# Kernel tuning notes

Measured on AMD Instinct MI355X. Metric: run time of the kernel, lower is better.

Reference implementation:

```python
import jax, jax.numpy as jnp
import numpy as np

KCODES = 512
BETA = 0.25   # beta_k = beta_v
GAMMA = 0.25  # gamma_k = gamma_v


def _quantise(z, codebook):
    """EMAQuantiser.forward in eval mode. z: [..., d], codebook: [k, d]."""
    d = z.shape[-1]
    zf = z.reshape(-1, d)                                   # [N, d]
    z2 = jnp.sum(zf * zf, axis=1, keepdims=True)            # [N, 1]
    c2 = jnp.sum(codebook * codebook, axis=1)               # [k]
    logits = zf @ codebook.T                                # [N, k]
    dist = z2 + c2[None, :] - 2.0 * logits                  # [N, k]
    indices = jnp.argmin(dist, axis=1)                      # [N]
    z_q = codebook[indices].reshape(z.shape)
    z_q_st = z + jax.lax.stop_gradient(z_q - z)
    loss_commit = jnp.mean((jax.lax.stop_gradient(z_q) - z) ** 2)
    loss_embed = jnp.mean((z_q - jax.lax.stop_gradient(z)) ** 2)
    counts = jax.ops.segment_sum(jnp.ones_like(indices, dtype=z.dtype), indices,
                                 num_segments=codebook.shape[0])
    usage = counts / jnp.maximum(counts.sum(), 1.0)
    return z_q_st, indices.reshape(z.shape[:-1]), loss_commit, loss_embed, usage


def setup_inputs() -> dict:
    key = jax.random.key(0)
    k1, k2, k3, k4 = jax.random.split(key, 4)
    B, H, S, D = 2, 16, 4096, 128
    return {
        "K": jax.random.normal(k1, (B, H, S, D), dtype=jnp.float32),
        "V": jax.random.normal(k2, (B, H, S, D), dtype=jnp.float32),
        "codebook_k": jax.random.normal(k3, (KCODES, D), dtype=jnp.float32) * 0.02,
        "codebook_v": jax.random.normal(k4, (KCODES, D), dtype=jnp.float32) * 0.02,
        "step": 20000,
    }


def reference(K, V, codebook_k, codebook_v, step):
    K_q, idx_k, commit_k, embed_k, usage_k = _quantise(K, codebook_k)
    V_q, idx_v, commit_v, embed_v, usage_v = _quantise(V, codebook_v)
    # eval mode: gates = ones -> mix == quantised straight-through values
    gates = jnp.ones_like(K[..., :1])
    K_mix = (1.0 - gates) * K + gates * K_q
    V_mix = (1.0 - gates) * V + gates * V_q
    return (K_mix, V_mix,
            BETA * commit_k, BETA * commit_v,
            GAMMA * embed_k, GAMMA * embed_v,
            usage_k, usage_v)
```

## Files before the change

### kernel.cpp

```cpp
#include <hip/hip_runtime.h>
#include <hip/hip_fp16.h>

typedef _Float16 half8 __attribute__((ext_vector_type(8)));
typedef float floatx4 __attribute__((ext_vector_type(4)));

#define R_TOT   131072
#define OUT_SC  33554432
#define OUT_USE 33554436
#define WS_C2   524288
#define WS_IDX  528384
#define WS_LOSS 1576960


__global__ void vq_init(const float* __restrict__ cb_k, const float* __restrict__ cb_v,
                        float* __restrict__ out, char* __restrict__ ws) {
    const int b = blockIdx.x, t = threadIdx.x;
    if (b < 64) {
        const int tensor = b >> 5, nt = b & 31;
        const int s = t >> 6, lane = t & 63, l15 = lane & 15, quad = lane >> 4;
        const float* cb = tensor ? cb_v : cb_k;
        half8* wsh = (half8*)(ws + (size_t)tensor * 262144);
        half8* wsl = wsh + 8192;
        const int code = nt * 16 + l15;
        const float* src = cb + code * 128 + s * 32 + quad * 8;
        float4 z0 = *(const float4*)src;
        float4 z1 = *(const float4*)(src + 4);
        float zz[8] = {z0.x, z0.y, z0.z, z0.w, z1.x, z1.y, z1.z, z1.w};
        half8 h, l;
        float p = 0.0f;
        #pragma unroll
        for (int j = 0; j < 8; ++j) {
            _Float16 hi = (_Float16)zz[j];
            h[j] = hi;
            l[j] = (_Float16)((zz[j] - (float)hi) * 2048.0f);
            p = fmaf(zz[j], zz[j], p);
        }
        wsh[(nt * 4 + s) * 64 + lane] = h;
        wsl[(nt * 4 + s) * 64 + lane] = l;
        p += __shfl_xor(p, 16);
        p += __shfl_xor(p, 32);
        __shared__ float c2p[4][16];
        if (lane < 16) c2p[s][lane] = p;
        __syncthreads();
        if (t < 16)
            ((float*)(ws + WS_C2))[tensor * 512 + nt * 16 + t] =
                ((c2p[0][t] + c2p[1][t]) + c2p[2][t]) + c2p[3][t];
    } else {
        int i = (b - 64) * 256 + t;
        if (i < 1028) out[OUT_SC + i] = 0.0f;
    }
}

__global__ __launch_bounds__(256, 2)
void vq_main(const float* __restrict__ Kp, const float* __restrict__ Vp,
             const float* __restrict__ cb_k, const float* __restrict__ cb_v,
             float* __restrict__ out, char* __restrict__ ws) {
    __shared__ int   lds_idx[128];
    __shared__ float lds_loss[4];

    const int tid  = threadIdx.x;
    const int wave = tid >> 6;
    const int lane = tid & 63;
    const int quad = lane >> 4;
    const int l15  = lane & 15;
    const int tensor = blockIdx.y;

    const float* __restrict__ Z   = tensor ? Vp : Kp;
    const float* __restrict__ cbf = tensor ? cb_v : cb_k;
    const half8* __restrict__ gh  = (const half8*)(ws + (size_t)tensor * 262144);
    const half8* __restrict__ gl  = gh + 8192;
    const float* __restrict__ c2g = (const float*)(ws + WS_C2) + tensor * 512;
    int* __restrict__ idxg = (int*)(ws + WS_IDX) + tensor * R_TOT;
    float* __restrict__ lossp = (float*)(ws + WS_LOSS) + tensor * 2048;
    float* __restrict__ outz = out + (size_t)tensor * 16777216;

    const int blockRow = blockIdx.x * 128;
    const int waveRow  = blockRow + wave * 32;

    half8 ah[2][4], al[2][4];
    float z2r[2][4];
    #pragma unroll
    for (int t = 0; t < 2; ++t) {
        const float* zp = Z + (size_t)(waveRow + t * 16 + l15) * 128;
        float zsq = 0.0f;
        #pragma unroll
        for (int s = 0; s < 4; ++s) {
            const float* p = zp + s * 32 + quad * 8;
            float4 z0 = *(const float4*)p;
            float4 z1 = *(const float4*)(p + 4);
            float zz[8] = {z0.x, z0.y, z0.z, z0.w, z1.x, z1.y, z1.z, z1.w};
            #pragma unroll
            for (int j = 0; j < 8; ++j) {
                _Float16 h = (_Float16)zz[j];
                ah[t][s][j] = h;
                al[t][s][j] = (_Float16)((zz[j] - (float)h) * 2048.0f);
                zsq = fmaf(zz[j], zz[j], zsq);
            }
        }
        zsq += __shfl_xor(zsq, 16);
        zsq += __shfl_xor(zsq, 32);
        #pragma unroll
        for (int r = 0; r < 4; ++r) z2r[t][r] = __shfl(zsq, quad * 4 + r);
    }

    float bd[2][4];
    int   bi[2][4];
    #pragma unroll
    for (int t = 0; t < 2; ++t)
        #pragma unroll
        for (int r = 0; r < 4; ++r) { bd[t][r] = 3.4e38f; bi[t][r] = 0; }

    half8 bh[2][4], bl[2][4];
    #pragma unroll
    for (int s = 0; s < 4; ++s) {
        bh[0][s] = gh[s * 64 + lane];
        bl[0][s] = gl[s * 64 + lane];
    }

    #pragma unroll 2
    for (int nt = 0; nt < 32; ++nt) {
        const int cur = nt & 1, nxt = cur ^ 1;
        if (nt < 31) {
            #pragma unroll
            for (int s = 0; s < 4; ++s) {
                bh[nxt][s] = gh[((nt + 1) * 4 + s) * 64 + lane];
                bl[nxt][s] = gl[((nt + 1) * 4 + s) * 64 + lane];
            }
        }
        const float c2v = c2g[nt * 16 + l15];
        floatx4 p10 = {0,0,0,0}, p11 = {0,0,0,0}, p20 = {0,0,0,0}, p21 = {0,0,0,0};
        #pragma unroll
        for (int s = 0; s < 4; ++s) {
            p10 = __builtin_amdgcn_mfma_f32_16x16x32_f16(ah[0][s], bh[cur][s], p10, 0, 0, 0);
            p11 = __builtin_amdgcn_mfma_f32_16x16x32_f16(ah[1][s], bh[cur][s], p11, 0, 0, 0);
            p20 = __builtin_amdgcn_mfma_f32_16x16x32_f16(al[0][s], bh[cur][s], p20, 0, 0, 0);
            p21 = __builtin_amdgcn_mfma_f32_16x16x32_f16(al[1][s], bh[cur][s], p21, 0, 0, 0);
            p20 = __builtin_amdgcn_mfma_f32_16x16x32_f16(ah[0][s], bl[cur][s], p20, 0, 0, 0);
            p21 = __builtin_amdgcn_mfma_f32_16x16x32_f16(ah[1][s], bl[cur][s], p21, 0, 0, 0);
        }
        const int codeg = nt * 16 + l15;
        #pragma unroll
        for (int r = 0; r < 4; ++r) {
            float lg0 = fmaf(p20[r], 0x1p-11f, p10[r]);
            float d0  = fmaf(-2.0f, lg0, z2r[0][r] + c2v);
            if (d0 < bd[0][r]) { bd[0][r] = d0; bi[0][r] = codeg; }
            float lg1 = fmaf(p21[r], 0x1p-11f, p11[r]);
            float d1  = fmaf(-2.0f, lg1, z2r[1][r] + c2v);
            if (d1 < bd[1][r]) { bd[1][r] = d1; bi[1][r] = codeg; }
        }
    }

    float lp = 0.0f;
    #pragma unroll
    for (int t = 0; t < 2; ++t)
        #pragma unroll
        for (int r = 0; r < 4; ++r) {
            float d = bd[t][r];
            int   i = bi[t][r];
            #pragma unroll
            for (int off = 8; off; off >>= 1) {
                float od = __shfl_xor(d, off);
                int   oi = __shfl_xor(i, off);
                if (od < d || (od == d && oi < i)) { d = od; i = oi; }
            }
            if (l15 == 0) {
                lds_idx[wave * 32 + t * 16 + quad * 4 + r] = i;
                lp += d;
            }
        }
    lp += __shfl_xor(lp, 16);
    lp += __shfl_xor(lp, 32);
    if (lane == 0) lds_loss[wave] = lp;
    __syncthreads();

    if (tid == 0) {
        float bsum = ((lds_loss[0] + lds_loss[1]) + lds_loss[2]) + lds_loss[3];
        lossp[blockIdx.x] = bsum * 0x1p-26f;
    }
    if (tid < 128) idxg[blockRow + tid] = lds_idx[tid];

    #pragma unroll
    for (int g = 0; g < 16; ++g) {
        int rl  = g * 8 + (tid >> 5);
        int idx = lds_idx[rl];
        int col = (tid & 31) * 4;
        float4 v = *(const float4*)(cbf + idx * 128 + col);
        *(float4*)(outz + (size_t)(blockRow + rl) * 128 + col) = v;
    }
}

__global__ void vq_hist(const char* __restrict__ ws, float* __restrict__ out) {
    const int tid = threadIdx.x;
    const int b = blockIdx.x;
    if (b < 16) {
        __shared__ int h[512];
        const int tensor = b >> 3;
        const int seg = b & 7;
        h[tid] = 0; h[tid + 256] = 0;
        __syncthreads();
        const int* p = (const int*)(ws + WS_IDX) + tensor * R_TOT + seg * 16384;
        #pragma unroll
        for (int r = 0; r < 64; ++r) atomicAdd(&h[p[r * 256 + tid]], 1);
        __syncthreads();
        int c0 = h[tid], c1 = h[tid + 256];
        if (c0) atomicAdd(&out[OUT_USE + tensor * 512 + tid], (float)c0 * 0x1p-17f);
        if (c1) atomicAdd(&out[OUT_USE + tensor * 512 + tid + 256], (float)c1 * 0x1p-17f);
    } else {
        const int tensor = b - 16;
        const float* lossp = (const float*)(ws + WS_LOSS) + tensor * 2048;
        float s = 0.0f;
        #pragma unroll
        for (int j = 0; j < 8; ++j) s += lossp[j * 256 + tid];
        #pragma unroll
        for (int off = 1; off < 64; off <<= 1) s += __shfl_xor(s, off);
        __shared__ float l4[4];
        if ((tid & 63) == 0) l4[tid >> 6] = s;
        __syncthreads();
        if (tid == 0) {
            float tot = ((l4[0] + l4[1]) + l4[2]) + l4[3];
            out[OUT_SC + tensor] = tot;
            out[OUT_SC + 2 + tensor] = tot;
        }
    }
}

extern "C" void kernel_launch(void* const* d_in, const int* in_sizes, int n_in,
                              void* d_out, int out_size, void* d_ws, size_t ws_size,
                              hipStream_t stream) {
    (void)in_sizes; (void)n_in; (void)out_size; (void)ws_size;
    const float* K   = (const float*)d_in[0];
    const float* V   = (const float*)d_in[1];
    const float* cbk = (const float*)d_in[2];
    const float* cbv = (const float*)d_in[3];
    float* out = (float*)d_out;
    char* ws = (char*)d_ws;
    hipLaunchKernelGGL(vq_init, dim3(69), dim3(256), 0, stream, cbk, cbv, out, ws);
    hipLaunchKernelGGL(vq_main, dim3(1024, 2), dim3(256), 0, stream, K, V, cbk, cbv, out, ws);
    hipLaunchKernelGGL(vq_hist, dim3(18), dim3(256), 0, stream, (const char*)ws, out);
}
```

Before: 326.0 us.

## Stage codebook tiles through LDS with async global_load_lds ring buffer

Each block now shares the fp16 hi/lo codebook tiles through a 4-slot LDS ring buffer filled with direct global-to-LDS loads three tiles ahead, instead of every wave loading them from global into registers. The c2 norms are also staged in LDS. The aim is to cut redundant per-wave global traffic and register pressure in the distance loop, at the cost of a block-wide barrier per tile and hand-coded vmcnt waits. Separately, the histogram kernel is split across more blocks to spread the LDS atomics.

```diff
diff --git a/kernel.cpp b/kernel.cpp
--- a/kernel.cpp
+++ b/kernel.cpp
@@ -51,10 +51,18 @@
     }
 }
 
+__device__ __forceinline__ void gload_lds16(const void* g, void* l) {
+    __builtin_amdgcn_global_load_lds(
+        (const __attribute__((address_space(1))) void*)g,
+        (__attribute__((address_space(3))) void*)l, 16, 0, 0);
+}
+
 __global__ __launch_bounds__(256, 2)
 void vq_main(const float* __restrict__ Kp, const float* __restrict__ Vp,
              const float* __restrict__ cb_k, const float* __restrict__ cb_v,
              float* __restrict__ out, char* __restrict__ ws) {
+    __shared__ half8 buf[4][512];
+    __shared__ float c2s[512];
     __shared__ int   lds_idx[128];
     __shared__ float lds_loss[4];
 
@@ -76,6 +84,14 @@
 
     const int blockRow = blockIdx.x * 128;
     const int waveRow  = blockRow + wave * 32;
+
+    #pragma unroll
+    for (int pc = 0; pc < 3; ++pc) {
+        gload_lds16(gh + pc * 256 + tid, &buf[pc][tid]);
+        gload_lds16(gl + pc * 256 + tid, &buf[pc][256 + tid]);
+    }
+    c2s[tid]       = c2g[tid];
+    c2s[tid + 256] = c2g[tid + 256];
 
     half8 ah[2][4], al[2][4];
     float z2r[2][4];
@@ -110,45 +126,54 @@
         #pragma unroll
         for (int r = 0; r < 4; ++r) { bd[t][r] = 3.4e38f; bi[t][r] = 0; }
 
-    half8 bh[2][4], bl[2][4];
-    #pragma unroll
-    for (int s = 0; s < 4; ++s) {
-        bh[0][s] = gh[s * 64 + lane];
-        bl[0][s] = gl[s * 64 + lane];
-    }
-
-    #pragma unroll 2
-    for (int nt = 0; nt < 32; ++nt) {
-        const int cur = nt & 1, nxt = cur ^ 1;
-        if (nt < 31) {
-            #pragma unroll
-            for (int s = 0; s < 4; ++s) {
-                bh[nxt][s] = gh[((nt + 1) * 4 + s) * 64 + lane];
-                bl[nxt][s] = gl[((nt + 1) * 4 + s) * 64 + lane];
-            }
-        }
-        const float c2v = c2g[nt * 16 + l15];
-        floatx4 p10 = {0,0,0,0}, p11 = {0,0,0,0}, p20 = {0,0,0,0}, p21 = {0,0,0,0};
-        #pragma unroll
-        for (int s = 0; s < 4; ++s) {
-            p10 = __builtin_amdgcn_mfma_f32_16x16x32_f16(ah[0][s], bh[cur][s], p10, 0, 0, 0);
-            p11 = __builtin_amdgcn_mfma_f32_16x16x32_f16(ah[1][s], bh[cur][s], p11, 0, 0, 0);
-            p20 = __builtin_amdgcn_mfma_f32_16x16x32_f16(al[0][s], bh[cur][s], p20, 0, 0, 0);
-            p21 = __builtin_amdgcn_mfma_f32_16x16x32_f16(al[1][s], bh[cur][s], p21, 0, 0, 0);
-            p20 = __builtin_amdgcn_mfma_f32_16x16x32_f16(ah[0][s], bl[cur][s], p20, 0, 0, 0);
-            p21 = __builtin_amdgcn_mfma_f32_16x16x32_f16(ah[1][s], bl[cur][s], p21, 0, 0, 0);
-        }
-        const int codeg = nt * 16 + l15;
-        #pragma unroll
-        for (int r = 0; r < 4; ++r) {
-            float lg0 = fmaf(p20[r], 0x1p-11f, p10[r]);
-            float d0  = fmaf(-2.0f, lg0, z2r[0][r] + c2v);
-            if (d0 < bd[0][r]) { bd[0][r] = d0; bi[0][r] = codeg; }
-            float lg1 = fmaf(p21[r], 0x1p-11f, p11[r]);
-            float d1  = fmaf(-2.0f, lg1, z2r[1][r] + c2v);
-            if (d1 < bd[1][r]) { bd[1][r] = d1; bi[1][r] = codeg; }
-        }
-    }
+    asm volatile("s_waitcnt lgkmcnt(0)" ::: "memory");
+
+#define KSTEP(NT_, WAITS_)                                                        \
+    {                                                                             \
+        const int nt = (NT_);                                                     \
+        asm volatile(WAITS_ ::: "memory");                                        \
+        asm volatile("s_barrier" ::: "memory");                                   \
+        if (nt < 29) {                                                            \
+            const int pc = nt + 3;                                                \
+            gload_lds16(gh + pc * 256 + tid, &buf[pc & 3][tid]);                  \
+            gload_lds16(gl + pc * 256 + tid, &buf[pc & 3][256 + tid]);            \
+        }                                                                         \
+        const half8* bp = buf[nt & 3];                                            \
+        half8 bh[4], bl[4];                                                       \
+        _Pragma("unroll")                                                         \
+        for (int s = 0; s < 4; ++s) {            \
+            bh[s] = bp[s * 64 + lane];                                            \
+            bl[s] = bp[256 + s * 64 + lane];                                      \
+        }                                                                         \
+        const float c2v = c2s[nt * 16 + l15];                                     \
+        floatx4 p10 = {0,0,0,0}, p11 = {0,0,0,0}, p20 = {0,0,0,0}, p21 = {0,0,0,0};\
+        _Pragma("unroll")                                                         \
+        for (int s = 0; s < 4; ++s) {                                             \
+            p10 = __builtin_amdgcn_mfma_f32_16x16x32_f16(ah[0][s], bh[s], p10, 0, 0, 0); \
+            p11 = __builtin_amdgcn_mfma_f32_16x16x32_f16(ah[1][s], bh[s], p11, 0, 0, 0); \
+            p20 = __builtin_amdgcn_mfma_f32_16x16x32_f16(al[0][s], bh[s], p20, 0, 0, 0); \
+            p21 = __builtin_amdgcn_mfma_f32_16x16x32_f16(al[1][s], bh[s], p21, 0, 0, 0); \
+            p20 = __builtin_amdgcn_mfma_f32_16x16x32_f16(ah[0][s], bl[s], p20, 0, 0, 0); \
+            p21 = __builtin_amdgcn_mfma_f32_16x16x32_f16(ah[1][s], bl[s], p21, 0, 0, 0); \
+        }                                                                         \
+        const int codeg = nt * 16 + l15;                                          \
+         \
+        _Pragma("unroll")                                                         \
+        for (int r = 0; r < 4; ++r) {                                             \
+            float lg0 = fmaf(p20[r], 0x1p-11f, p10[r]);                           \
+            float d0  = fmaf(-2.0f, lg0, z2r[0][r] + c2v);                        \
+            if (d0 < bd[0][r]) { bd[0][r] = d0; bi[0][r] = codeg; }               \
+            float lg1 = fmaf(p21[r], 0x1p-11f, p11[r]);                           \
+            float d1  = fmaf(-2.0f, lg1, z2r[1][r] + c2v);                        \
+            if (d1 < bd[1][r]) { bd[1][r] = d1; bi[1][r] = codeg; }               \
+        }                                                                         \
+    }
+
+    for (int ntv = 0; ntv < 30; ++ntv)
+        KSTEP(ntv, "s_waitcnt vmcnt(4)");
+    KSTEP(30, "s_waitcnt vmcnt(2)");
+    KSTEP(31, "s_waitcnt vmcnt(0)");
+#undef KSTEP
 
     float lp = 0.0f;
     #pragma unroll
@@ -192,21 +217,21 @@
 __global__ void vq_hist(const char* __restrict__ ws, float* __restrict__ out) {
     const int tid = threadIdx.x;
     const int b = blockIdx.x;
-    if (b < 16) {
+    if (b < 64) {
         __shared__ int h[512];
-        const int tensor = b >> 3;
-        const int seg = b & 7;
+        const int tensor = b >> 5;
+        const int seg = b & 31;
         h[tid] = 0; h[tid + 256] = 0;
         __syncthreads();
-        const int* p = (const int*)(ws + WS_IDX) + tensor * R_TOT + seg * 16384;
-        #pragma unroll
-        for (int r = 0; r < 64; ++r) atomicAdd(&h[p[r * 256 + tid]], 1);
+        const int* p = (const int*)(ws + WS_IDX) + tensor * R_TOT + seg * 4096;
+        #pragma unroll
+        for (int r = 0; r < 16; ++r) atomicAdd(&h[p[r * 256 + tid]], 1);
         __syncthreads();
         int c0 = h[tid], c1 = h[tid + 256];
         if (c0) atomicAdd(&out[OUT_USE + tensor * 512 + tid], (float)c0 * 0x1p-17f);
         if (c1) atomicAdd(&out[OUT_USE + tensor * 512 + tid + 256], (float)c1 * 0x1p-17f);
     } else {
-        const int tensor = b - 16;
+        const int tensor = b - 64;
         const float* lossp = (const float*)(ws + WS_LOSS) + tensor * 2048;
         float s = 0.0f;
         #pragma unroll
@@ -236,5 +261,5 @@
     char* ws = (char*)d_ws;
     hipLaunchKernelGGL(vq_init, dim3(69), dim3(256), 0, stream, cbk, cbv, out, ws);
     hipLaunchKernelGGL(vq_main, dim3(1024, 2), dim3(256), 0, stream, K, V, cbk, cbv, out, ws);
-    hipLaunchKernelGGL(vq_hist, dim3(18), dim3(256), 0, stream, (const char*)ws, out);
-}
+    hipLaunchKernelGGL(vq_hist, dim3(66), dim3(256), 0, stream, (const char*)ws, out);
+}
```

New measurement: 334.9 us. +2.8%, slower.
